# Kernel tuning notes

Measured on AMD Instinct MI355X. Metric: run time of the kernel, lower is better.

Reference implementation:

```python
import jax, jax.numpy as jnp
import numpy as np

NUM_HEADS = 8


def setup_inputs() -> dict:
    key = jax.random.key(0)
    ks = jax.random.split(key, 8)
    B, N, H, W = 8, 1024, 32, 32
    dim = H * W  # 1024
    x1 = jax.random.normal(ks[0], (B, N, H, W), dtype=jnp.float32)
    x2 = jax.random.normal(ks[1], (B, N, H, W), dtype=jnp.float32)
    conv_w = jax.random.normal(ks[2], (N, 2 * N, 3, 3), dtype=jnp.float32) * 0.01
    conv_b = jnp.zeros((N,), dtype=jnp.float32)
    wq = jax.random.normal(ks[3], (dim, dim), dtype=jnp.float32) * 0.02
    wk = jax.random.normal(ks[4], (dim, dim), dtype=jnp.float32) * 0.02
    wv = jax.random.normal(ks[5], (dim, dim), dtype=jnp.float32) * 0.02
    proj_w = jax.random.normal(ks[6], (dim, dim), dtype=jnp.float32) * 0.02
    proj_b = jnp.zeros((dim,), dtype=jnp.float32)
    return {"x1": x1, "x2": x2, "conv_w": conv_w, "conv_b": conv_b,
            "wq": wq, "wk": wk, "wv": wv, "proj_w": proj_w, "proj_b": proj_b}


def reference(x1, x2, conv_w, conv_b, wq, wk, wv, proj_w, proj_b):
    B, N, H, W = x1.shape
    C = H * W
    nh = NUM_HEADS
    hd = C // nh
    scale = hd ** -0.5

    # conv_cat: Conv2d(2N -> N, k=3, pad=1) on channel-concatenated inputs
    x_cat = jnp.concatenate([x1, x2], axis=1)  # [B, 2N, H, W]
    x_cat = jax.lax.conv_general_dilated(
        x_cat, conv_w, window_strides=(1, 1), padding=((1, 1), (1, 1)),
        dimension_numbers=("NCHW", "OIHW", "NCHW"))
    x_cat = x_cat + conv_b[None, :, None, None]
    x_cat = x_cat.reshape(B, N, C)  # [B, N, C]

    # torch Linear: y = x @ W.T (no bias, qkv_bias=False)
    def heads(t):  # [B, N, C] -> [B, nh, N, hd]
        return t.reshape(B, N, nh, hd).transpose(0, 2, 1, 3)

    q = heads(x1.reshape(B, N, C) @ wq.T)
    k = heads(x_cat @ wk.T)
    v = heads(x_cat @ wv.T)

    # attention: softmax(q k^T * scale) v   (dropout is identity at p=0)
    attn = jnp.einsum("bhnd,bhmd->bhnm", q, k) * scale
    attn = jax.nn.softmax(attn, axis=-1)
    x_attn = jnp.einsum("bhnm,bhmd->bhnd", attn, v)  # [B, nh, N, hd]
    x_attn = x_attn.transpose(0, 2, 1, 3).reshape(B, N, C)

    out = (x_attn @ proj_w.T + proj_b).reshape(B, N, H, W) + x1
    return out
```

## Files before the change

### kernel.cpp

```cpp
#include <hip/hip_runtime.h>
#include <hip/hip_bf16.h>
#include <cstdint>
#include <cstddef>

typedef __attribute__((ext_vector_type(8))) short short8;
typedef __attribute__((ext_vector_type(4))) float f32x4;
typedef unsigned short u16;

static __device__ __forceinline__ u16 f2bf(float f) {
  __hip_bfloat16 h = __float2bfloat16(f);
  return *reinterpret_cast<u16*>(&h);
}

static __device__ __forceinline__ void gload16(const void* g, void* l) {
  __builtin_amdgcn_global_load_lds(
      (const __attribute__((address_space(1))) void*)g,
      (__attribute__((address_space(3))) void*)l, 16, 0, 0);
}


__global__ void cast_k(const float* __restrict__ in, u16* __restrict__ out, int n4) {
  int i = blockIdx.x * 256 + threadIdx.x;
  if (i < n4) {
    float4 v = ((const float4*)in)[i];
    union { u16 u[4]; uint2 p; } r;
    r.u[0] = f2bf(v.x); r.u[1] = f2bf(v.y); r.u[2] = f2bf(v.z); r.u[3] = f2bf(v.w);
    ((uint2*)out)[i] = r.p;
  }
}

__global__ void build_int(const float* __restrict__ x1, const float* __restrict__ x2,
                          u16* __restrict__ in_t) {
  __shared__ float tile[64][65];
  const int it = blockIdx.x;
  const int st = blockIdx.y;
  const int b  = blockIdx.z;
  const int i0 = it * 64, s0 = st * 64;
  const float* src = (i0 < 1024)
      ? x1 + ((size_t)b * 1024 + i0) * 1024
      : x2 + ((size_t)b * 1024 + (i0 - 1024)) * 1024;
  const int t = threadIdx.x;
  #pragma unroll
  for (int jj = 0; jj < 16; ++jj) {
    int idx = jj * 256 + t;
    int ii = idx >> 6, si = idx & 63;
    tile[ii][si] = src[(size_t)ii * 1024 + s0 + si];
  }
  __syncthreads();
  #pragma unroll
  for (int jj = 0; jj < 16; ++jj) {
    int idx = jj * 256 + t;
    int si = idx >> 6, ii = idx & 63;
    in_t[((size_t)b * 1024 + s0 + si) * 2048 + i0 + ii] = f2bf(tile[ii][si]);
  }
}

__global__ void pack_wp(const float* __restrict__ cw, u16* __restrict__ Wp) {
  __shared__ float sb[2304];
  const int blk = blockIdx.x;
  const int t = threadIdx.x;
  const size_t base = (size_t)blk * 2304;
  #pragma unroll
  for (int jj = 0; jj < 9; ++jj) sb[jj * 256 + t] = cw[base + jj * 256 + t];
  __syncthreads();
  const int p = blk * 256 + t;
  #pragma unroll
  for (int q = 0; q < 9; ++q)
    Wp[(size_t)q * 2097152 + p] = f2bf(sb[t * 9 + q]);
}

__global__ void zero_k(u16* z) { z[threadIdx.x] = 0; }


enum { GM_PLAIN = 0, GM_VT = 1, GM_PROJ = 2, GM_CONV = 3 };

template<int MODE>
__global__ __launch_bounds__(512, 2)
void gemm3_k(const u16* __restrict__ A, const u16* __restrict__ B,
             u16* __restrict__ Cb, float* __restrict__ Cf,
             const float* __restrict__ bias, const float* __restrict__ resid,
             const u16* __restrict__ zb, int Ktot) {
  __shared__ u16 lds[3 * 24576];
  const int tid = threadIdx.x;
  const int lane = tid & 63;
  const int w = tid >> 6;
  const int l15 = lane & 15, l4 = lane >> 4;

  const int bid = blockIdx.x;
  const int lb = (bid & 7) * 32 + (bid >> 3);
  const int tm = lb >> 3, tn = lb & 7;
  const int row0 = tm * 256, col0 = tn * 128;
  const int wr = (w >> 1) * 64, wc = (w & 1) * 64;

  const int sr = w * 8 + (lane >> 3);
  const int pp = (lane & 7) ^ (lane >> 3);

  int am[4], ay[4], ax[4];
  #pragma unroll
  for (int u = 0; u < 4; ++u) {
    const int m = row0 + u * 64 + sr;
    am[u] = m;
    const int s = m & 1023;
    ay[u] = s >> 5; ax[u] = s & 31;
  }

  f32x4 acc[4][4];
  #pragma unroll
  for (int i = 0; i < 4; ++i)
    #pragma unroll
    for (int jj = 0; jj < 4; ++jj)
      acc[i][jj] = (f32x4){0.f, 0.f, 0.f, 0.f};

  const int nK = Ktot >> 6;

  auto stage = [&](int kt, u16* buf) {
    u16* da = buf + (size_t)w * 512;
    u16* db = buf + 16384 + (size_t)w * 512;
    if constexpr (MODE == GM_CONV) {
      const int q = kt >> 5;
      const int ks = (kt & 31) << 6;
      const int qd = (q >= 6) ? 2 : (q >= 3) ? 1 : 0;
      const int dy = qd - 1, dx = q - qd * 3 - 1;
      const int dd = (dy << 5) + dx;
      #pragma unroll
      for (int u = 0; u < 4; ++u) {
        const int yy = ay[u] + dy, xx = ax[u] + dx;
        const bool valid = ((unsigned)yy < 32u) && ((unsigned)xx < 32u);
        const u16* ga = valid ? A + (((size_t)(am[u] + dd)) << 11) + ks + pp * 8 : zb;
        gload16(ga, da + u * 4096);
      }
      const size_t boff = ((size_t)q << 21) + ks + pp * 8;
      #pragma unroll
      for (int u = 0; u < 2; ++u) {
        const u16* gb = B + boff + ((size_t)(col0 + u * 64 + sr) << 11);
        gload16(gb, db + u * 4096);
      }
    } else {
      const int k0 = kt << 6;
      #pragma unroll
      for (int u = 0; u < 4; ++u) {
        const u16* ga = A + (size_t)(row0 + u * 64 + sr) * Ktot + k0 + pp * 8;
        gload16(ga, da + u * 4096);
      }
      #pragma unroll
      for (int u = 0; u < 2; ++u) {
        const u16* gb = B + (size_t)(col0 + u * 64 + sr) * Ktot + k0 + pp * 8;
        gload16(gb, db + u * 4096);
      }
    }
  };

  auto compute = [&](const u16* buf) {
    const char* Ar = (const char*)buf;
    const char* Br = (const char*)(buf + 16384);
    #pragma unroll
    for (int ks = 0; ks < 2; ++ks) {
      const int bcol = ((ks << 6) + (l4 << 4)) ^ ((l15 & 7) << 4);
      short8 av[4], bv[4];
      #pragma unroll
      for (int mi = 0; mi < 4; ++mi)
        av[mi] = *(const short8*)(Ar + (wr + mi * 16 + l15) * 128 + bcol);
      #pragma unroll
      for (int ni = 0; ni < 4; ++ni)
        bv[ni] = *(const short8*)(Br + (wc + ni * 16 + l15) * 128 + bcol);
      __builtin_amdgcn_s_setprio(1);
      #pragma unroll
      for (int mi = 0; mi < 4; ++mi)
        #pragma unroll
        for (int ni = 0; ni < 4; ++ni)
          acc[mi][ni] = __builtin_amdgcn_mfma_f32_16x16x32_bf16(av[mi], bv[ni], acc[mi][ni], 0, 0, 0);
      __builtin_amdgcn_s_setprio(0);
    }
  };

  u16* pb0 = lds;
  u16* pb1 = lds + 24576;
  u16* pb2 = lds + 49152;

  stage(0, pb0);
  stage(1, pb1);
  for (int t = 0; t < nK; ++t) {
    if (t + 1 < nK) {
      asm volatile("s_waitcnt vmcnt(6)" ::: "memory");
    } else {
      asm volatile("s_waitcnt vmcnt(0)" ::: "memory");
    }
    __builtin_amdgcn_s_barrier();
    if (t + 2 < nK) stage(t + 2, pb2);
    compute(pb0);
    u16* tmp = pb0; pb0 = pb1; pb1 = pb2; pb2 = tmp;
  }

  #pragma unroll
  for (int mi = 0; mi < 4; ++mi) {
    #pragma unroll
    for (int ni = 0; ni < 4; ++ni) {
      #pragma unroll
      for (int j = 0; j < 4; ++j) {
        const int grow = row0 + wr + mi * 16 + l4 * 4 + j;
        const int gcol = col0 + wc + ni * 16 + l15;
        const float v = acc[mi][ni][j];
        if constexpr (MODE == GM_PLAIN) {
          Cb[((size_t)grow << 10) + gcol] = f2bf(v);
        } else if constexpr (MODE == GM_VT) {
          const int b = grow >> 10, ms = grow & 1023;
          const int h = gcol >> 7, d = gcol & 127;
          Cb[((size_t)((b * 8 + h) * 128 + d) << 10) + ms] = f2bf(v);
        } else if constexpr (MODE == GM_PROJ) {
          const size_t o = ((size_t)grow << 10) + gcol;
          Cf[o] = v + bias[gcol] + resid[o];
        } else {
          const int b = grow >> 10, s = grow & 1023;
          Cb[((size_t)((b << 10) + gcol) << 10) + s] = f2bf(v + bias[gcol]);
        }
      }
    }
  }
}

__global__ __launch_bounds__(256, 2)
void attn_k(const u16* __restrict__ Q, const u16* __restrict__ K,
            const u16* __restrict__ Vt, u16* __restrict__ O) {
  __shared__ u16 Ks[64 * 128];
  __shared__ u16 Vs[128 * 64];
  __shared__ u16 Plds[4][16 * 80];
  const int mtile = blockIdx.x;
  const int bh = blockIdx.y;
  const int b = bh >> 3, h = bh & 7;
  const int tid = threadIdx.x, lane = tid & 63, w = tid >> 6;
  const int l15 = lane & 15, l4 = lane >> 4;

  short8 qf[4];
  {
    const int qrow = b * 1024 + mtile * 64 + w * 16 + l15;
    const u16* qb = Q + ((size_t)qrow << 10) + h * 128;
    #pragma unroll
    for (int kk = 0; kk < 4; ++kk)
      qf[kk] = *(const short8*)(qb + kk * 32 + l4 * 8);
  }

  f32x4 o[8];
  #pragma unroll
  for (int db = 0; db < 8; ++db) o[db] = (f32x4){0.f, 0.f, 0.f, 0.f};
  float mrow[4], lrow[4];
  #pragma unroll
  for (int j = 0; j < 4; ++j) { mrow[j] = -1e30f; lrow[j] = 0.f; }
  const float scale = 0.08838834764831845f;

  for (int kt = 0; kt < 16; ++kt) {
    __syncthreads();
    #pragma unroll
    for (int j = 0; j < 4; ++j) {
      const int c = (j * 4 + w) * 64 + lane;
      const int r = c >> 4, coff = (c & 15) << 3;
      const u16* gp = K + ((size_t)(b * 1024 + kt * 64 + r) << 10) + h * 128 + coff;
      gload16(gp, (void*)(Ks + (j * 4 + w) * 512));
    }
    #pragma unroll
    for (int j = 0; j < 4; ++j) {
      const int c = (j * 4 + w) * 64 + lane;
      const int r = c >> 3, coff = (c & 7) << 3;
      const u16* gp = Vt + ((size_t)((b * 8 + h) * 128 + r) << 10) + kt * 64 + coff;
      gload16(gp, (void*)(Vs + (j * 4 + w) * 512));
    }
    __syncthreads();
    f32x4 s[4];
    #pragma unroll
    for (int cb = 0; cb < 4; ++cb) {
      s[cb] = (f32x4){0.f, 0.f, 0.f, 0.f};
      #pragma unroll
      for (int kk = 0; kk < 4; ++kk) {
        short8 bK = *(const short8*)(Ks + (cb * 16 + l15) * 128 + kk * 32 + l4 * 8);
        s[cb] = __builtin_amdgcn_mfma_f32_16x16x32_bf16(qf[kk], bK, s[cb], 0, 0, 0);
      }
    }
    #pragma unroll
    for (int cb = 0; cb < 4; ++cb) {
      s[cb][0] *= scale; s[cb][1] *= scale; s[cb][2] *= scale; s[cb][3] *= scale;
    }
    #pragma unroll
    for (int j = 0; j < 4; ++j) {
      float mx = fmaxf(fmaxf(s[0][j], s[1][j]), fmaxf(s[2][j], s[3][j]));
      #pragma unroll
      for (int off = 8; off >= 1; off >>= 1)
        mx = fmaxf(mx, __shfl_xor(mx, off, 64));
      const float mn = fmaxf(mrow[j], mx);
      const float fac = __expf(mrow[j] - mn);
      mrow[j] = mn;
      float rs = 0.f;
      #pragma unroll
      for (int cb = 0; cb < 4; ++cb) {
        const float p = __expf(s[cb][j] - mn);
        s[cb][j] = p;
        rs += p;
      }
      #pragma unroll
      for (int off = 8; off >= 1; off >>= 1)
        rs += __shfl_xor(rs, off, 64);
      lrow[j] = lrow[j] * fac + rs;
      #pragma unroll
      for (int db = 0; db < 8; ++db) o[db][j] *= fac;
    }
    u16* pl = Plds[w];
    #pragma unroll
    for (int cb = 0; cb < 4; ++cb)
      #pragma unroll
      for (int j = 0; j < 4; ++j)
        pl[(l4 * 4 + j) * 80 + cb * 16 + l15] = f2bf(s[cb][j]);
    __syncthreads();
    short8 ap[2];
    #pragma unroll
    for (int ks = 0; ks < 2; ++ks)
      ap[ks] = *(const short8*)(pl + l15 * 80 + ks * 32 + l4 * 8);
    #pragma unroll
    for (int db = 0; db < 8; ++db) {
      #pragma unroll
      for (int ks = 0; ks < 2; ++ks) {
        short8 bV = *(const short8*)(Vs + (db * 16 + l15) * 64 + ks * 32 + l4 * 8);
        o[db] = __builtin_amdgcn_mfma_f32_16x16x32_bf16(ap[ks], bV, o[db], 0, 0, 0);
      }
    }
  }
  #pragma unroll
  for (int db = 0; db < 8; ++db) {
    #pragma unroll
    for (int j = 0; j < 4; ++j) {
      const int grow = b * 1024 + mtile * 64 + w * 16 + l4 * 4 + j;
      const int gcol = h * 128 + db * 16 + l15;
      O[((size_t)grow << 10) + gcol] = f2bf(o[db][j] / lrow[j]);
    }
  }
}


extern "C" void kernel_launch(void* const* d_in, const int* in_sizes, int n_in,
                              void* d_out, int out_size, void* d_ws, size_t ws_size,
                              hipStream_t stream) {
  const float* x1     = (const float*)d_in[0];
  const float* x2     = (const float*)d_in[1];
  const float* conv_w = (const float*)d_in[2];
  const float* conv_b = (const float*)d_in[3];
  const float* wq     = (const float*)d_in[4];
  const float* wk     = (const float*)d_in[5];
  const float* wv     = (const float*)d_in[6];
  const float* proj_w = (const float*)d_in[7];
  const float* proj_b = (const float*)d_in[8];
  float* out = (float*)d_out;

  char* ws = (char*)d_ws;
  size_t off = 0;
  auto alloc = [&](size_t bytes) -> void* {
    void* p = ws + off;
    off += (bytes + 255) & ~(size_t)255;
    return p;
  };
  u16* x1b  = (u16*)alloc(8192ULL * 1024 * 2);
  u16* in_t = (u16*)alloc(8ULL * 1024 * 2048 * 2);
  u16* Wp   = (u16*)alloc(9ULL * 2097152 * 2);
  u16* wqb  = (u16*)alloc(1048576ULL * 2);
  u16* wkb  = (u16*)alloc(1048576ULL * 2);
  u16* wvb  = (u16*)alloc(1048576ULL * 2);
  u16* pjb  = (u16*)alloc(1048576ULL * 2);
  u16* xc   = (u16*)alloc(8192ULL * 1024 * 2);
  u16* Qb   = (u16*)alloc(8192ULL * 1024 * 2);
  u16* Kb   = (u16*)alloc(8192ULL * 1024 * 2);
  u16* Vtb  = (u16*)alloc(8192ULL * 1024 * 2);
  u16* Ob   = (u16*)alloc(8192ULL * 1024 * 2);
  u16* zb   = (u16*)alloc(256);

  cast_k<<<8192, 256, 0, stream>>>(x1, x1b, 2097152);
  cast_k<<<1024, 256, 0, stream>>>(wq, wqb, 262144);
  cast_k<<<1024, 256, 0, stream>>>(wk, wkb, 262144);
  cast_k<<<1024, 256, 0, stream>>>(wv, wvb, 262144);
  cast_k<<<1024, 256, 0, stream>>>(proj_w, pjb, 262144);
  build_int<<<dim3(32, 16, 8), 256, 0, stream>>>(x1, x2, in_t);
  pack_wp<<<8192, 256, 0, stream>>>(conv_w, Wp);
  zero_k<<<1, 128, 0, stream>>>(zb);

  gemm3_k<GM_CONV><<<256, 512, 0, stream>>>(in_t, Wp, xc, nullptr, conv_b, nullptr, zb, 18432);
  gemm3_k<GM_PLAIN><<<256, 512, 0, stream>>>(x1b, wqb, Qb, nullptr, nullptr, nullptr, zb, 1024);
  gemm3_k<GM_PLAIN><<<256, 512, 0, stream>>>(xc, wkb, Kb, nullptr, nullptr, nullptr, zb, 1024);
  gemm3_k<GM_VT><<<256, 512, 0, stream>>>(xc, wvb, Vtb, nullptr, nullptr, nullptr, zb, 1024);
  attn_k<<<dim3(16, 64), 256, 0, stream>>>(Qb, Kb, Vtb, Ob);
  gemm3_k<GM_PROJ><<<256, 512, 0, stream>>>(Ob, pjb, nullptr, out, proj_b, x1, zb, 1024);
}
```

Measured before the change: 591.8 us.

## Split GEMM k-step staging, fuse K/V GEMMs, double-buffer attention K/V

The GEMM main loop is split into two half-k substeps. Global-to-LDS staging of the next A and B tiles is spread across them, with extra barriers, explicit lgkmcnt waits and sched barriers so loads overlap the MFMA work. The K and V projections become one GEMM launched on 512 workgroups, which writes K row-major and V transposed. This relies on the wk and wv bf16 buffers sitting next to each other in the workspace. The attention kernel double-buffers its K/V LDS tiles with an XOR swizzle to cut bank conflicts, and replaces one __syncthreads with a wave-local lgkmcnt wait; the extra barriers in the GEMM could cost some throughput.

```diff
diff --git a/kernel.cpp b/kernel.cpp
--- a/kernel.cpp
+++ b/kernel.cpp
@@ -72,23 +72,25 @@
 __global__ void zero_k(u16* z) { z[threadIdx.x] = 0; }
 
 
-enum { GM_PLAIN = 0, GM_VT = 1, GM_PROJ = 2, GM_CONV = 3 };
+enum { GM_PLAIN = 0, GM_VT = 1, GM_PROJ = 2, GM_CONV = 3, GM_KV = 4 };
 
 template<int MODE>
 __global__ __launch_bounds__(512, 2)
-void gemm3_k(const u16* __restrict__ A, const u16* __restrict__ B,
-             u16* __restrict__ Cb, float* __restrict__ Cf,
+void gemm4_k(const u16* __restrict__ A, const u16* __restrict__ B,
+             u16* __restrict__ Cb, u16* __restrict__ Cb2, float* __restrict__ Cf,
              const float* __restrict__ bias, const float* __restrict__ resid,
-             const u16* __restrict__ zb, int Ktot) {
+             const u16* __restrict__ zb, int Ktot, int ntn_sh) {
   __shared__ u16 lds[3 * 24576];
   const int tid = threadIdx.x;
   const int lane = tid & 63;
   const int w = tid >> 6;
   const int l15 = lane & 15, l4 = lane >> 4;
 
+  const int nwg = gridDim.x;
   const int bid = blockIdx.x;
-  const int lb = (bid & 7) * 32 + (bid >> 3);
-  const int tm = lb >> 3, tn = lb & 7;
+  const int lb = (bid & 7) * (nwg >> 3) + (bid >> 3);
+  const int tm = lb >> ntn_sh;
+  const int tn = lb & ((1 << ntn_sh) - 1);
   const int row0 = tm * 256, col0 = tn * 128;
   const int wr = (w >> 1) * 64, wc = (w & 1) * 64;
 
@@ -113,23 +115,46 @@
 
   const int nK = Ktot >> 6;
 
-  auto stage = [&](int kt, u16* buf) {
+  auto stageA = [&](int kt, u16* buf) {
+    u16* da = buf + (size_t)w * 512;
+    if constexpr (MODE == GM_CONV) {
+      const int q = kt >> 5;
+      const int ks0 = (kt & 31) << 6;
+      const int qd = (q >= 6) ? 2 : (q >= 3) ? 1 : 0;
+      const int dy = qd - 1, dx = q - qd * 3 - 1;
+      const int dd = (dy << 5) + dx;
+      #pragma unroll
+      for (int u = 0; u < 3; ++u) {
+        const int yy = ay[u] + dy, xx = ax[u] + dx;
+        const bool valid = ((unsigned)yy < 32u) && ((unsigned)xx < 32u);
+        const u16* ga = valid ? A + (((size_t)(am[u] + dd)) << 11) + ks0 + pp * 8 : zb;
+        gload16(ga, da + u * 4096);
+      }
+    } else {
+      const int k0 = kt << 6;
+      #pragma unroll
+      for (int u = 0; u < 3; ++u) {
+        const u16* ga = A + (size_t)(row0 + u * 64 + sr) * Ktot + k0 + pp * 8;
+        gload16(ga, da + u * 4096);
+      }
+    }
+  };
+  auto stageB = [&](int kt, u16* buf) {
     u16* da = buf + (size_t)w * 512;
     u16* db = buf + 16384 + (size_t)w * 512;
     if constexpr (MODE == GM_CONV) {
       const int q = kt >> 5;
-      const int ks = (kt & 31) << 6;
+      const int ks0 = (kt & 31) << 6;
       const int qd = (q >= 6) ? 2 : (q >= 3) ? 1 : 0;
       const int dy = qd - 1, dx = q - qd * 3 - 1;
       const int dd = (dy << 5) + dx;
-      #pragma unroll
-      for (int u = 0; u < 4; ++u) {
-        const int yy = ay[u] + dy, xx = ax[u] + dx;
+      {
+        const int yy = ay[3] + dy, xx = ax[3] + dx;
         const bool valid = ((unsigned)yy < 32u) && ((unsigned)xx < 32u);
-        const u16* ga = valid ? A + (((size_t)(am[u] + dd)) << 11) + ks + pp * 8 : zb;
-        gload16(ga, da + u * 4096);
-      }
-      const size_t boff = ((size_t)q << 21) + ks + pp * 8;
+        const u16* ga = valid ? A + (((size_t)(am[3] + dd)) << 11) + ks0 + pp * 8 : zb;
+        gload16(ga, da + 3 * 4096);
+      }
+      const size_t boff = ((size_t)q << 21) + ks0 + pp * 8;
       #pragma unroll
       for (int u = 0; u < 2; ++u) {
         const u16* gb = B + boff + ((size_t)(col0 + u * 64 + sr) << 11);
@@ -137,10 +162,9 @@
       }
     } else {
       const int k0 = kt << 6;
-      #pragma unroll
-      for (int u = 0; u < 4; ++u) {
-        const u16* ga = A + (size_t)(row0 + u * 64 + sr) * Ktot + k0 + pp * 8;
-        gload16(ga, da + u * 4096);
+      {
+        const u16* ga = A + (size_t)(row0 + 3 * 64 + sr) * Ktot + k0 + pp * 8;
+        gload16(ga, da + 3 * 4096);
       }
       #pragma unroll
       for (int u = 0; u < 2; ++u) {
@@ -150,12 +174,20 @@
     }
   };
 
-  auto compute = [&](const u16* buf) {
-    const char* Ar = (const char*)buf;
-    const char* Br = (const char*)(buf + 16384);
-    #pragma unroll
-    for (int ks = 0; ks < 2; ++ks) {
-      const int bcol = ((ks << 6) + (l4 << 4)) ^ ((l15 & 7) << 4);
+  u16* pb0 = lds;
+  u16* pb1 = lds + 24576;
+  u16* pb2 = lds + 49152;
+
+  stageA(0, pb0); stageB(0, pb0);
+  stageA(1, pb1); stageB(1, pb1);
+  asm volatile("s_waitcnt vmcnt(6)" ::: "memory");
+  __builtin_amdgcn_s_barrier();
+
+  for (int t = 0; t < nK; ++t) {
+    const char* Ar = (const char*)pb0;
+    const char* Br = (const char*)(pb0 + 16384);
+    {
+      const int bcol = (l4 << 4) ^ ((l15 & 7) << 4);
       short8 av[4], bv[4];
       #pragma unroll
       for (int mi = 0; mi < 4; ++mi)
@@ -163,6 +195,10 @@
       #pragma unroll
       for (int ni = 0; ni < 4; ++ni)
         bv[ni] = *(const short8*)(Br + (wc + ni * 16 + l15) * 128 + bcol);
+      if (t + 2 < nK) stageA(t + 2, pb2);
+      __builtin_amdgcn_s_barrier();
+      asm volatile("s_waitcnt lgkmcnt(0)" ::: "memory");
+      __builtin_amdgcn_sched_barrier(0);
       __builtin_amdgcn_s_setprio(1);
       #pragma unroll
       for (int mi = 0; mi < 4; ++mi)
@@ -170,24 +206,35 @@
         for (int ni = 0; ni < 4; ++ni)
           acc[mi][ni] = __builtin_amdgcn_mfma_f32_16x16x32_bf16(av[mi], bv[ni], acc[mi][ni], 0, 0, 0);
       __builtin_amdgcn_s_setprio(0);
-    }
-  };
-
-  u16* pb0 = lds;
-  u16* pb1 = lds + 24576;
-  u16* pb2 = lds + 49152;
-
-  stage(0, pb0);
-  stage(1, pb1);
-  for (int t = 0; t < nK; ++t) {
-    if (t + 1 < nK) {
-      asm volatile("s_waitcnt vmcnt(6)" ::: "memory");
-    } else {
-      asm volatile("s_waitcnt vmcnt(0)" ::: "memory");
-    }
-    __builtin_amdgcn_s_barrier();
-    if (t + 2 < nK) stage(t + 2, pb2);
-    compute(pb0);
+      __builtin_amdgcn_s_barrier();
+    }
+    {
+      const int bcol = (64 + (l4 << 4)) ^ ((l15 & 7) << 4);
+      short8 av[4], bv[4];
+      #pragma unroll
+      for (int mi = 0; mi < 4; ++mi)
+        av[mi] = *(const short8*)(Ar + (wr + mi * 16 + l15) * 128 + bcol);
+      #pragma unroll
+      for (int ni = 0; ni < 4; ++ni)
+        bv[ni] = *(const short8*)(Br + (wc + ni * 16 + l15) * 128 + bcol);
+      if (t + 2 < nK) {
+        stageB(t + 2, pb2);
+        asm volatile("s_waitcnt vmcnt(6)" ::: "memory");
+      } else if (t + 1 < nK) {
+        asm volatile("s_waitcnt vmcnt(0)" ::: "memory");
+      }
+      __builtin_amdgcn_s_barrier();
+      asm volatile("s_waitcnt lgkmcnt(0)" ::: "memory");
+      __builtin_amdgcn_sched_barrier(0);
+      __builtin_amdgcn_s_setprio(1);
+      #pragma unroll
+      for (int mi = 0; mi < 4; ++mi)
+        #pragma unroll
+        for (int ni = 0; ni < 4; ++ni)
+          acc[mi][ni] = __builtin_amdgcn_mfma_f32_16x16x32_bf16(av[mi], bv[ni], acc[mi][ni], 0, 0, 0);
+      __builtin_amdgcn_s_setprio(0);
+      __builtin_amdgcn_s_barrier();
+    }
     u16* tmp = pb0; pb0 = pb1; pb1 = pb2; pb2 = tmp;
   }
 
@@ -206,6 +253,15 @@
           const int b = grow >> 10, ms = grow & 1023;
           const int h = gcol >> 7, d = gcol & 127;
           Cb[((size_t)((b * 8 + h) * 128 + d) << 10) + ms] = f2bf(v);
+        } else if constexpr (MODE == GM_KV) {
+          if (gcol < 1024) {
+            Cb[((size_t)grow << 10) + gcol] = f2bf(v);
+          } else {
+            const int c = gcol - 1024;
+            const int b = grow >> 10, ms = grow & 1023;
+            const int h = c >> 7, d = c & 127;
+            Cb2[((size_t)((b * 8 + h) * 128 + d) << 10) + ms] = f2bf(v);
+          }
         } else if constexpr (MODE == GM_PROJ) {
           const size_t o = ((size_t)grow << 10) + gcol;
           Cf[o] = v + bias[gcol] + resid[o];
@@ -219,10 +275,10 @@
 }
 
 __global__ __launch_bounds__(256, 2)
-void attn_k(const u16* __restrict__ Q, const u16* __restrict__ K,
-            const u16* __restrict__ Vt, u16* __restrict__ O) {
-  __shared__ u16 Ks[64 * 128];
-  __shared__ u16 Vs[128 * 64];
+void attn2_k(const u16* __restrict__ Q, const u16* __restrict__ K,
+             const u16* __restrict__ Vt, u16* __restrict__ O) {
+  __shared__ u16 Ks[2][64 * 128];
+  __shared__ u16 Vs[2][128 * 64];
   __shared__ u16 Plds[4][16 * 80];
   const int mtile = blockIdx.x;
   const int bh = blockIdx.y;
@@ -247,30 +303,42 @@
   for (int j = 0; j < 4; ++j) { mrow[j] = -1e30f; lrow[j] = 0.f; }
   const float scale = 0.08838834764831845f;
 
-  for (int kt = 0; kt < 16; ++kt) {
-    __syncthreads();
+  auto stageKV = [&](int kt, int half) {
     #pragma unroll
     for (int j = 0; j < 4; ++j) {
       const int c = (j * 4 + w) * 64 + lane;
-      const int r = c >> 4, coff = (c & 15) << 3;
+      const int r = c >> 4;
+      const int coff = (((c & 15) ^ (r & 7)) << 3);
       const u16* gp = K + ((size_t)(b * 1024 + kt * 64 + r) << 10) + h * 128 + coff;
-      gload16(gp, (void*)(Ks + (j * 4 + w) * 512));
+      gload16(gp, (void*)(Ks[half] + (j * 4 + w) * 512));
     }
     #pragma unroll
     for (int j = 0; j < 4; ++j) {
       const int c = (j * 4 + w) * 64 + lane;
-      const int r = c >> 3, coff = (c & 7) << 3;
+      const int r = c >> 3;
+      const int coff = (((c & 7) ^ (r & 7)) << 3);
       const u16* gp = Vt + ((size_t)((b * 8 + h) * 128 + r) << 10) + kt * 64 + coff;
-      gload16(gp, (void*)(Vs + (j * 4 + w) * 512));
-    }
-    __syncthreads();
+      gload16(gp, (void*)(Vs[half] + (j * 4 + w) * 512));
+    }
+  };
+
+  stageKV(0, 0);
+  for (int kt = 0; kt < 16; ++kt) {
+    const int cur = kt & 1;
+    asm volatile("s_waitcnt vmcnt(0)" ::: "memory");
+    __builtin_amdgcn_s_barrier();
+    if (kt + 1 < 16) stageKV(kt + 1, cur ^ 1);
+
+    const u16* ks_ = Ks[cur];
+    const u16* vs_ = Vs[cur];
     f32x4 s[4];
     #pragma unroll
     for (int cb = 0; cb < 4; ++cb) {
       s[cb] = (f32x4){0.f, 0.f, 0.f, 0.f};
       #pragma unroll
       for (int kk = 0; kk < 4; ++kk) {
-        short8 bK = *(const short8*)(Ks + (cb * 16 + l15) * 128 + kk * 32 + l4 * 8);
+        const int col = (kk * 32 + l4 * 8) ^ ((l15 & 7) << 3);
+        short8 bK = *(const short8*)(ks_ + (cb * 16 + l15) * 128 + col);
         s[cb] = __builtin_amdgcn_mfma_f32_16x16x32_bf16(qf[kk], bK, s[cb], 0, 0, 0);
       }
     }
@@ -307,17 +375,19 @@
       #pragma unroll
       for (int j = 0; j < 4; ++j)
         pl[(l4 * 4 + j) * 80 + cb * 16 + l15] = f2bf(s[cb][j]);
-    __syncthreads();
+    asm volatile("s_waitcnt lgkmcnt(0)" ::: "memory");
+    __builtin_amdgcn_sched_barrier(0);
     short8 ap[2];
     #pragma unroll
-    for (int ks = 0; ks < 2; ++ks)
-      ap[ks] = *(const short8*)(pl + l15 * 80 + ks * 32 + l4 * 8);
+    for (int ks2 = 0; ks2 < 2; ++ks2)
+      ap[ks2] = *(const short8*)(pl + l15 * 80 + ks2 * 32 + l4 * 8);
     #pragma unroll
     for (int db = 0; db < 8; ++db) {
       #pragma unroll
-      for (int ks = 0; ks < 2; ++ks) {
-        short8 bV = *(const short8*)(Vs + (db * 16 + l15) * 64 + ks * 32 + l4 * 8);
-        o[db] = __builtin_amdgcn_mfma_f32_16x16x32_bf16(ap[ks], bV, o[db], 0, 0, 0);
+      for (int ks2 = 0; ks2 < 2; ++ks2) {
+        const int col = (ks2 * 32 + l4 * 8) ^ ((l15 & 7) << 3);
+        short8 bV = *(const short8*)(vs_ + (db * 16 + l15) * 64 + col);
+        o[db] = __builtin_amdgcn_mfma_f32_16x16x32_bf16(ap[ks2], bV, o[db], 0, 0, 0);
       }
     }
   }
@@ -377,10 +447,9 @@
   pack_wp<<<8192, 256, 0, stream>>>(conv_w, Wp);
   zero_k<<<1, 128, 0, stream>>>(zb);
 
-  gemm3_k<GM_CONV><<<256, 512, 0, stream>>>(in_t, Wp, xc, nullptr, conv_b, nullptr, zb, 18432);
-  gemm3_k<GM_PLAIN><<<256, 512, 0, stream>>>(x1b, wqb, Qb, nullptr, nullptr, nullptr, zb, 1024);
-  gemm3_k<GM_PLAIN><<<256, 512, 0, stream>>>(xc, wkb, Kb, nullptr, nullptr, nullptr, zb, 1024);
-  gemm3_k<GM_VT><<<256, 512, 0, stream>>>(xc, wvb, Vtb, nullptr, nullptr, nullptr, zb, 1024);
-  attn_k<<<dim3(16, 64), 256, 0, stream>>>(Qb, Kb, Vtb, Ob);
-  gemm3_k<GM_PROJ><<<256, 512, 0, stream>>>(Ob, pjb, nullptr, out, proj_b, x1, zb, 1024);
-}
+  gemm4_k<GM_CONV><<<256, 512, 0, stream>>>(in_t, Wp, xc, nullptr, nullptr, conv_b, nullptr, zb, 18432, 3);
+  gemm4_k<GM_PLAIN><<<256, 512, 0, stream>>>(x1b, wqb, Qb, nullptr, nullptr, nullptr, nullptr, zb, 1024, 3);
+  gemm4_k<GM_KV><<<512, 512, 0, stream>>>(xc, wkb, Kb, Vtb, nullptr, nullptr, nullptr, zb, 1024, 4);
+  attn2_k<<<dim3(16, 64), 256, 0, stream>>>(Qb, Kb, Vtb, Ob);
+  gemm4_k<GM_PROJ><<<256, 512, 0, stream>>>(Ob, pjb, nullptr, nullptr, out, proj_b, x1, zb, 1024, 3);
+}
```

New measurement: 604.3 us. +2.1%, slower.
